# Performance work log

Measured on AMD Instinct MI355X. Metric: run time of the kernel, lower is better.

The kernel has to match this reference:

```python
import jax, jax.numpy as jnp
import numpy as np

C = 256      # channel_num
K = 9        # key_num
B, H, W = 8, 64, 64


def setup_inputs() -> dict:
    key = jax.random.key(0)
    ks = jax.random.split(key, 12)
    s = 1.0 / np.sqrt(C)
    return {
        "query_layer": jax.random.normal(ks[0], (B, C, H, W), jnp.float32),
        "key_layer": jax.random.normal(ks[1], (B, C, H, W), jnp.float32),
        "gumbel_noise": jax.random.gumbel(ks[2], (B, K, H, W), jnp.float32),
        "w_refer": jax.random.normal(ks[3], (C, C), jnp.float32) * s,
        "b_refer": jax.random.normal(ks[4], (C,), jnp.float32) * 0.01,
        "w_attn": jax.random.normal(ks[5], (K, C), jnp.float32) * s,
        "b_attn": jax.random.normal(ks[6], (K,), jnp.float32) * 0.01,
        "w_mask": jax.random.normal(ks[7], (K, C), jnp.float32) * s,
        "b_mask": jax.random.normal(ks[8], (K,), jnp.float32) * 0.01,
        "w_off": jax.random.normal(ks[9], (2 * K, C), jnp.float32) * 0.02,
        "b_off": jax.random.normal(ks[10], (2 * K,), jnp.float32) * 0.01,
        "temp": 1,
    }


def _conv1x1(w, b, x):
    # w: (O,C), x: (B,C,H,W) -> (B,O,H,W)
    return jnp.einsum('oc,bchw->bohw', w, x) + b[None, :, None, None]


def _sample_one(img, py, px):
    # img: (C,H,W); py,px: (K,H,W) absolute sampling coords (bilinear, zero pad)
    h, w = img.shape[1], img.shape[2]
    y0 = jnp.floor(py)
    x0 = jnp.floor(px)
    wy = py - y0          # weight toward y0+1
    wx = px - x0

    def gather(yi, xi):
        valid = (yi >= 0) & (yi < h) & (xi >= 0) & (xi < w)
        yc = jnp.clip(yi, 0, h - 1).astype(jnp.int32)
        xc = jnp.clip(xi, 0, w - 1).astype(jnp.int32)
        return img[:, yc, xc] * valid[None].astype(img.dtype)  # (C,K,H,W)

    out = (gather(y0, x0) * ((1 - wy) * (1 - wx))[None]
           + gather(y0, x0 + 1) * ((1 - wy) * wx)[None]
           + gather(y0 + 1, x0) * (wy * (1 - wx))[None]
           + gather(y0 + 1, x0 + 1) * (wy * wx)[None])
    return out  # (C,K,H,W)


def reference(query_layer, key_layer, gumbel_noise, w_refer, b_refer,
              w_attn, b_attn, w_mask, b_mask, w_off, b_off, temp):
    key_feature = _conv1x1(w_refer, b_refer, key_layer)          # (B,C,H,W)
    attn_weights = _conv1x1(w_attn, b_attn, query_layer)         # (B,K,H,W)
    soft_mask = _conv1x1(w_mask, b_mask, query_layer)            # (B,K,H,W)
    # gumbel_softmax(hard=False) over key dim
    hard_mask = jax.nn.softmax((soft_mask + gumbel_noise) / temp, axis=1)
    offset = _conv1x1(w_off, b_off, query_layer)                 # (B,2K,H,W)

    # faithful to offset[:, i:i+2]: overlapping (dy,dx) slices
    dy = offset[:, 0:K]        # (B,K,H,W)
    dx = offset[:, 1:K + 1]    # (B,K,H,W)
    ys = jnp.arange(H, dtype=offset.dtype)[None, None, :, None]
    xs = jnp.arange(W, dtype=offset.dtype)[None, None, None, :]
    py = ys + dy
    px = xs + dx

    sampled = jax.vmap(_sample_one)(key_feature, py, px)         # (B,C,K,H,W)

    aw = jax.nn.softmax(attn_weights * hard_mask, axis=1)        # (B,K,H,W)
    out = jnp.einsum('bkhw,bckhw->bchw', aw, sampled)            # (B,C,H,W)
    return out
```

## Files before the change

kernel.cpp:

```cpp
#include <hip/hip_runtime.h>

typedef unsigned short u16;
typedef __attribute__((ext_vector_type(8))) short bf16x8;
typedef __attribute__((ext_vector_type(4))) float f32x4;

__device__ __forceinline__ u16 f2bf(float f) {
    unsigned u = __float_as_uint(f);
    unsigned r = (u + 0x7fffu + ((u >> 16) & 1u)) >> 16;
    return (u16)r;
}
__device__ __forceinline__ float bf2f(u16 h) {
    union { unsigned u; float f; } x; x.u = ((unsigned)h) << 16; return x.f;
}

#define NB 8
#define NC 256
#define NK 9
#define NH 64
#define NW 64
#define NP 4096
#define BAND 320
#define SB_STRIDE 328
#define KS_STRIDE 264

__global__ __launch_bounds__(256) void kf_gemm(const float* __restrict__ key,
                                               const float* __restrict__ w_refer,
                                               const float* __restrict__ b_refer,
                                               u16* __restrict__ kf16)
{
    __shared__ u16 K_s[64 * KS_STRIDE];
    const int bid = blockIdx.x;
    const int b   = bid >> 6;
    const int p0  = (bid & 63) << 6;
    const int t = threadIdx.x;
    const int lane = t & 63, wid = t >> 6;
    const int fr = lane & 15, kq = (lane >> 4) << 3;
    const int co0w = wid << 6;

    #pragma unroll
    for (int rep = 0; rep < 16; ++rep) {
        int k = (rep << 4) + (t >> 4), px4 = (t & 15) << 2;
        float4 v = *(const float4*)&key[((size_t)b * NC + k) * NP + p0 + px4];
        K_s[(px4 + 0) * KS_STRIDE + k] = f2bf(v.x);
        K_s[(px4 + 1) * KS_STRIDE + k] = f2bf(v.y);
        K_s[(px4 + 2) * KS_STRIDE + k] = f2bf(v.z);
        K_s[(px4 + 3) * KS_STRIDE + k] = f2bf(v.w);
    }
    __syncthreads();

    f32x4 acc[4][4];
    #pragma unroll
    for (int i = 0; i < 4; ++i)
        #pragma unroll
        for (int j = 0; j < 4; ++j) acc[i][j] = (f32x4){0.f, 0.f, 0.f, 0.f};

    for (int ks = 0; ks < 8; ++ks) {
        const int k0 = (ks << 5) + kq;
        bf16x8 af[4], bfv[4];
        #pragma unroll
        for (int mi = 0; mi < 4; ++mi) {
            const float* src = &w_refer[(size_t)(co0w + (mi << 4) + fr) * NC + k0];
            float4 v0 = *(const float4*)src;
            float4 v1 = *(const float4*)(src + 4);
            bf16x8 a;
            a[0] = (short)f2bf(v0.x); a[1] = (short)f2bf(v0.y);
            a[2] = (short)f2bf(v0.z); a[3] = (short)f2bf(v0.w);
            a[4] = (short)f2bf(v1.x); a[5] = (short)f2bf(v1.y);
            a[6] = (short)f2bf(v1.z); a[7] = (short)f2bf(v1.w);
            af[mi] = a;
        }
        #pragma unroll
        for (int ni = 0; ni < 4; ++ni)
            bfv[ni] = *(const bf16x8*)&K_s[((ni << 4) + fr) * KS_STRIDE + k0];
        #pragma unroll
        for (int mi = 0; mi < 4; ++mi)
            #pragma unroll
            for (int ni = 0; ni < 4; ++ni)
                acc[mi][ni] = __builtin_amdgcn_mfma_f32_16x16x32_bf16(af[mi], bfv[ni], acc[mi][ni], 0, 0, 0);
    }
    const int col = lane & 15, rbase = (lane >> 4) << 2;
    #pragma unroll
    for (int mi = 0; mi < 4; ++mi) {
        #pragma unroll
        for (int rr = 0; rr < 4; ++rr) {
            int co = co0w + (mi << 4) + rbase + rr;
            float bias = b_refer[co];
            u16* dst = &kf16[((size_t)b * NC + co) * NP + p0 + col];
            #pragma unroll
            for (int ni = 0; ni < 4; ++ni)
                dst[ni << 4] = f2bf(acc[mi][ni][rr] + bias);
        }
    }
}

__global__ __launch_bounds__(256) void head_meta(const float* __restrict__ query,
                                                 const float* __restrict__ gumbel,
                                                 const float* __restrict__ w_attn, const float* __restrict__ b_attn,
                                                 const float* __restrict__ w_mask, const float* __restrict__ b_mask,
                                                 const float* __restrict__ w_off,  const float* __restrict__ b_off,
                                                 const int* __restrict__ temp_p,
                                                 float4* __restrict__ wgt, uint2* __restrict__ offs)
{
    __shared__ u16 A[48][264];
    __shared__ float hdT[128][41];
    const int pt = blockIdx.x;
    const int b  = pt >> 5;
    const int p0 = (pt & 31) << 7;
    const int t = threadIdx.x;
    const int lane = t & 63, wn = t >> 6;
    const int fr = lane & 15, kq = (lane >> 4) << 3;

    for (int i = t; i < 1152; i += 256) {
        int o = i >> 5, c = (i & 31) << 3;
        const float* src = (o < 9) ? &w_attn[o * NC + c]
                       : (o < 18 ? &w_mask[(o - 9) * NC + c]
                                 : &w_off[(o - 18) * NC + c]);
        float4 v0 = *(const float4*)src;
        float4 v1 = *(const float4*)(src + 4);
        bf16x8 a;
        a[0] = (short)f2bf(v0.x); a[1] = (short)f2bf(v0.y);
        a[2] = (short)f2bf(v0.z); a[3] = (short)f2bf(v0.w);
        a[4] = (short)f2bf(v1.x); a[5] = (short)f2bf(v1.y);
        a[6] = (short)f2bf(v1.z); a[7] = (short)f2bf(v1.w);
        *(bf16x8*)&A[o][c] = a;
    }
    for (int i = t; i < 384; i += 256) {
        bf16x8 z = {0,0,0,0,0,0,0,0};
        *(bf16x8*)&A[36 + (i >> 5)][(i & 31) << 3] = z;
    }
    __syncthreads();

    f32x4 acc[3][2];
    #pragma unroll
    for (int i = 0; i < 3; ++i)
        #pragma unroll
        for (int j = 0; j < 2; ++j) acc[i][j] = (f32x4){0.f, 0.f, 0.f, 0.f};

    for (int ks = 0; ks < 8; ++ks) {
        const int k0 = (ks << 5) + kq;
        bf16x8 af[3], bfv[2];
        #pragma unroll
        for (int mi = 0; mi < 3; ++mi)
            af[mi] = *(const bf16x8*)&A[(mi << 4) + fr][k0];
        #pragma unroll
        for (int ni = 0; ni < 2; ++ni) {
            const float* src = &query[((size_t)b * NC + k0) * NP + p0 + (wn << 5) + (ni << 4) + fr];
            bf16x8 bv;
            #pragma unroll
            for (int j = 0; j < 8; ++j) bv[j] = (short)f2bf(src[(size_t)j * NP]);
            bfv[ni] = bv;
        }
        #pragma unroll
        for (int mi = 0; mi < 3; ++mi)
            #pragma unroll
            for (int ni = 0; ni < 2; ++ni)
                acc[mi][ni] = __builtin_amdgcn_mfma_f32_16x16x32_bf16(af[mi], bfv[ni], acc[mi][ni], 0, 0, 0);
    }
    const int col = lane & 15, rbase = (lane >> 4) << 2;
    #pragma unroll
    for (int mi = 0; mi < 3; ++mi) {
        #pragma unroll
        for (int rr = 0; rr < 4; ++rr) {
            int o = (mi << 4) + rbase + rr;
            if (o < 36) {
                float bias = (o < 9) ? b_attn[o] : (o < 18) ? b_mask[o - 9] : b_off[o - 18];
                #pragma unroll
                for (int ni = 0; ni < 2; ++ni)
                    hdT[(wn << 5) + (ni << 4) + col][o] = acc[mi][ni][rr] + bias;
            }
        }
    }
    __syncthreads();

    if (t < 128) {
        const int pxg = p0 + t;
        const int row = pxg >> 6, xcol = pxg & 63;
        float v[36];
        #pragma unroll
        for (int o = 0; o < 36; ++o) v[o] = hdT[t][o];

        int ti = temp_p[0];
        float tempf = (ti >= 1 && ti < (1 << 23)) ? (float)ti : __int_as_float(ti);
        float am[9], hs[9];
        float mx = -1e30f;
        #pragma unroll
        for (int k = 0; k < 9; ++k) {
            am[k] = v[k];
            float g = gumbel[((size_t)b * NK + k) * NP + pxg];
            hs[k] = (v[9 + k] + g) / tempf;
            mx = fmaxf(mx, hs[k]);
        }
        float ssum = 0.f;
        #pragma unroll
        for (int k = 0; k < 9; ++k) { hs[k] = __expf(hs[k] - mx); ssum += hs[k]; }
        float inv = 1.f / ssum;
        float lg[9]; float mx2 = -1e30f;
        #pragma unroll
        for (int k = 0; k < 9; ++k) { lg[k] = am[k] * (hs[k] * inv); mx2 = fmaxf(mx2, lg[k]); }
        float s2 = 0.f;
        #pragma unroll
        for (int k = 0; k < 9; ++k) { lg[k] = __expf(lg[k] - mx2); s2 += lg[k]; }
        float inv2 = 1.f / s2;
        #pragma unroll
        for (int k = 0; k < 9; ++k) {
            float a = lg[k] * inv2;
            float pyv = (float)row  + v[18 + k];
            float pxv = (float)xcol + v[19 + k];
            float y0f = floorf(pyv), x0f = floorf(pxv);
            float wy = pyv - y0f, wx = pxv - x0f;
            int y0 = (int)y0f, x0 = (int)x0f;
            int y1 = y0 + 1, x1 = x0 + 1;
            float vy0 = (y0 >= 0 && y0 < NH) ? 1.f : 0.f;
            float vy1 = (y1 >= 0 && y1 < NH) ? 1.f : 0.f;
            float vx0 = (x0 >= 0 && x0 < NW) ? 1.f : 0.f;
            float vx1 = (x1 >= 0 && x1 < NW) ? 1.f : 0.f;
            int y0c = min(max(y0, 0), NH - 1), y1c = min(max(y1, 0), NH - 1);
            int x0c = min(max(x0, 0), NW - 1), x1c = min(max(x1, 0), NW - 1);
            unsigned o00 = (unsigned)(y0c * NW + x0c), o01 = (unsigned)(y0c * NW + x1c);
            unsigned o10 = (unsigned)(y1c * NW + x0c), o11 = (unsigned)(y1c * NW + x1c);
            size_t idx = ((size_t)b * NK + k) * NP + pxg;
            wgt[idx]  = make_float4(a * (1.f - wy) * (1.f - wx) * vy0 * vx0,
                                    a * (1.f - wy) * wx * vy0 * vx1,
                                    a * wy * (1.f - wx) * vy1 * vx0,
                                    a * wy * wx * vy1 * vx1);
            offs[idx] = make_uint2(o00 | (o01 << 16), o10 | (o11 << 16));
        }
    }
}

__global__ __launch_bounds__(512, 4) void sample_pass(const u16* __restrict__ kf16,
                                                      const float4* __restrict__ wgt,
                                                      const uint2* __restrict__ offs,
                                                      float* __restrict__ out)
{
    __shared__ float Sf[64][BAND];

    const int bid = blockIdx.x;
    const int b = bid & 7, row = bid >> 3;
    const int t = threadIdx.x;
    const int lane = t & 63, wid = t >> 6;
    const int fr = lane & 15, kq = (lane >> 4) << 3;
    const int c0 = wid << 5;
    const int ylo = min(max(row - 2, 0), NH - 5);
    const int base = ylo << 6;
    const u16* kfb = kf16 + (size_t)b * NC * NP + base;

    const int px = t & 63, kg = t >> 6;
    size_t idx0 = ((size_t)b * NK + kg) * NP + (row << 6) + px;
    float4 wv0 = wgt[idx0];
    uint2  ov0 = offs[idx0];
    float4 wv1 = make_float4(0.f, 0.f, 0.f, 0.f);
    uint2  ov1 = make_uint2(0u, 0u);
    if (kg == 0) {
        size_t idx1 = ((size_t)b * NK + 8) * NP + (row << 6) + px;
        wv1 = wgt[idx1]; ov1 = offs[idx1];
    }

    #pragma unroll
    for (int i = 0; i < 10; ++i)
        ((float4*)Sf)[t + (i << 9)] = (float4){0.f, 0.f, 0.f, 0.f};
    __syncthreads();

    bool esc = false;
    #pragma unroll
    for (int s = 0; s < 2; ++s) {
        if (s == 1 && kg != 0) break;
        float4 wv = s ? wv1 : wv0;
        uint2  ov = s ? ov1 : ov0;
        int   o4[4] = { (int)(ov.x & 0xffffu), (int)(ov.x >> 16),
                        (int)(ov.y & 0xffffu), (int)(ov.y >> 16) };
        float w4[4] = { wv.x, wv.y, wv.z, wv.w };
        #pragma unroll
        for (int c = 0; c < 4; ++c) {
            int u = o4[c] - base;
            if ((unsigned)u < (unsigned)BAND) atomicAdd(&Sf[px][u], w4[c]);
            else esc = true;
        }
    }
    __syncthreads();

    bf16x8 apre[4][2];
    #pragma unroll
    for (int s = 0; s < 4; ++s)
        #pragma unroll
        for (int mi = 0; mi < 2; ++mi)
            apre[s][mi] = *(const bf16x8*)&kfb[(size_t)(c0 + (mi << 4) + fr) * NP + (s << 5) + kq];

    u16* Sb = (u16*)&Sf[0][0];
    #pragma unroll
    for (int r = 0; r < 5; ++r) {
        int i = t + (r << 9);
        int p = i / 40, j = (i % 40) << 3;
        float4 a = *(const float4*)&Sf[p][j];
        float4 c = *(const float4*)&Sf[p][j + 4];
        bf16x8 q;
        q[0] = (short)f2bf(a.x); q[1] = (short)f2bf(a.y);
        q[2] = (short)f2bf(a.z); q[3] = (short)f2bf(a.w);
        q[4] = (short)f2bf(c.x); q[5] = (short)f2bf(c.y);
        q[6] = (short)f2bf(c.z); q[7] = (short)f2bf(c.w);
        __syncthreads();
        *(bf16x8*)&Sb[p * SB_STRIDE + j] = q;
    }
    __syncthreads();

    f32x4 acc[2][4];
    #pragma unroll
    for (int i = 0; i < 2; ++i)
        #pragma unroll
        for (int j = 0; j < 4; ++j) acc[i][j] = (f32x4){0.f, 0.f, 0.f, 0.f};

    #pragma unroll
    for (int step = 0; step < 10; ++step) {
        bf16x8 a0 = apre[step & 3][0], a1 = apre[step & 3][1];
        if (step + 4 < 10) {
            #pragma unroll
            for (int mi = 0; mi < 2; ++mi)
                apre[step & 3][mi] =
                    *(const bf16x8*)&kfb[(size_t)(c0 + (mi << 4) + fr) * NP + ((step + 4) << 5) + kq];
        }
        bf16x8 bfv[4];
        #pragma unroll
        for (int ni = 0; ni < 4; ++ni)
            bfv[ni] = *(const bf16x8*)&Sb[((ni << 4) + fr) * SB_STRIDE + (step << 5) + kq];
        #pragma unroll
        for (int ni = 0; ni < 4; ++ni) {
            acc[0][ni] = __builtin_amdgcn_mfma_f32_16x16x32_bf16(a0, bfv[ni], acc[0][ni], 0, 0, 0);
            acc[1][ni] = __builtin_amdgcn_mfma_f32_16x16x32_bf16(a1, bfv[ni], acc[1][ni], 0, 0, 0);
        }
    }

    const int col = lane & 15, rbase = (lane >> 4) << 2;
    float* ob = out + (size_t)b * NC * NP + (row << 6);
    #pragma unroll
    for (int mi = 0; mi < 2; ++mi) {
        #pragma unroll
        for (int rr = 0; rr < 4; ++rr) {
            int c = c0 + (mi << 4) + rbase + rr;
            #pragma unroll
            for (int ni = 0; ni < 4; ++ni)
                ob[(size_t)c * NP + (ni << 4) + col] = acc[mi][ni][rr];
        }
    }

    __syncthreads();
    if (esc) {
        for (int s = 0; s < (kg == 0 ? 2 : 1); ++s) {
            int k = s ? 8 : kg;
            size_t idx = ((size_t)b * NK + k) * NP + (row << 6) + px;
            float4 wv = wgt[idx];
            uint2  ov = offs[idx];
            int   o4[4] = { (int)(ov.x & 0xffffu), (int)(ov.x >> 16),
                            (int)(ov.y & 0xffffu), (int)(ov.y >> 16) };
            float w4[4] = { wv.x, wv.y, wv.z, wv.w };
            for (int c = 0; c < 4; ++c) {
                int u = o4[c] - base;
                if ((unsigned)u >= (unsigned)BAND) {
                    for (int cc = 0; cc < NC; ++cc)
                        atomicAdd(&ob[(size_t)cc * NP + px],
                                  w4[c] * bf2f(kf16[((size_t)b * NC + cc) * NP + o4[c]]));
                }
            }
        }
    }
}

extern "C" void kernel_launch(void* const* d_in, const int* in_sizes, int n_in,
                              void* d_out, int out_size, void* d_ws, size_t ws_size,
                              hipStream_t stream)
{
    const float* query   = (const float*)d_in[0];
    const float* key     = (const float*)d_in[1];
    const float* gumbel  = (const float*)d_in[2];
    const float* w_refer = (const float*)d_in[3];
    const float* b_refer = (const float*)d_in[4];
    const float* w_attn  = (const float*)d_in[5];
    const float* b_attn  = (const float*)d_in[6];
    const float* w_mask  = (const float*)d_in[7];
    const float* b_mask  = (const float*)d_in[8];
    const float* w_off   = (const float*)d_in[9];
    const float* b_off   = (const float*)d_in[10];
    const int*   temp    = (const int*)d_in[11];
    float* out = (float*)d_out;

    u16*    kf16 = (u16*)d_ws;
    float4* wgt  = (float4*)((char*)d_ws + (size_t)NB * NP * NC * 2);
    uint2*  offs = (uint2*)((char*)wgt + (size_t)NB * NK * NP * 16);

    kf_gemm<<<512, 256, 0, stream>>>(key, w_refer, b_refer, kf16);
    head_meta<<<256, 256, 0, stream>>>(query, gumbel, w_attn, b_attn, w_mask, b_mask,
                                       w_off, b_off, temp, wgt, offs);
    sample_pass<<<512, 512, 0, stream>>>(kf16, wgt, offs, out);
}
```

Before: 62.10 us.

## Drop LDS staging in kf_gemm, reorder block indexing, hoist prefetch, batch LDS repack

kf_gemm now reads key values straight from global memory into MFMA B fragments with strided scalar loads, removing the LDS transpose and its barrier. Block indices in kf_gemm and head_meta are remapped so consecutive blocks cover different batches. In sample_pass the kf16 A-fragment prefetch moves ahead of the scatter phase, and the bf16 repack collects all five chunks in registers before a single barrier instead of one barrier per chunk. The strided uncoalesced global reads in kf_gemm risk much lower memory efficiency, and the extra live registers may reduce occupancy.

```diff
diff --git a/kernel.cpp b/kernel.cpp
--- a/kernel.cpp
+++ b/kernel.cpp
@@ -21,38 +21,26 @@
 #define NP 4096
 #define BAND 320
 #define SB_STRIDE 328
-#define KS_STRIDE 264
 
 __global__ __launch_bounds__(256) void kf_gemm(const float* __restrict__ key,
                                                const float* __restrict__ w_refer,
                                                const float* __restrict__ b_refer,
                                                u16* __restrict__ kf16)
 {
-    __shared__ u16 K_s[64 * KS_STRIDE];
     const int bid = blockIdx.x;
-    const int b   = bid >> 6;
-    const int p0  = (bid & 63) << 6;
-    const int t = threadIdx.x;
-    const int lane = t & 63, wid = t >> 6;
+    const int b   = bid & 7;
+    const int p0  = (bid >> 3) << 6;
+    const int lane = threadIdx.x & 63, wid = threadIdx.x >> 6;
     const int fr = lane & 15, kq = (lane >> 4) << 3;
     const int co0w = wid << 6;
 
-    #pragma unroll
-    for (int rep = 0; rep < 16; ++rep) {
-        int k = (rep << 4) + (t >> 4), px4 = (t & 15) << 2;
-        float4 v = *(const float4*)&key[((size_t)b * NC + k) * NP + p0 + px4];
-        K_s[(px4 + 0) * KS_STRIDE + k] = f2bf(v.x);
-        K_s[(px4 + 1) * KS_STRIDE + k] = f2bf(v.y);
-        K_s[(px4 + 2) * KS_STRIDE + k] = f2bf(v.z);
-        K_s[(px4 + 3) * KS_STRIDE + k] = f2bf(v.w);
-    }
-    __syncthreads();
-
     f32x4 acc[4][4];
     #pragma unroll
     for (int i = 0; i < 4; ++i)
         #pragma unroll
         for (int j = 0; j < 4; ++j) acc[i][j] = (f32x4){0.f, 0.f, 0.f, 0.f};
+
+    const float* kb = &key[(size_t)b * NC * NP + p0];
 
     for (int ks = 0; ks < 8; ++ks) {
         const int k0 = (ks << 5) + kq;
@@ -70,14 +58,20 @@
             af[mi] = a;
         }
         #pragma unroll
-        for (int ni = 0; ni < 4; ++ni)
-            bfv[ni] = *(const bf16x8*)&K_s[((ni << 4) + fr) * KS_STRIDE + k0];
+        for (int ni = 0; ni < 4; ++ni) {
+            const float* src = &kb[(size_t)k0 * NP + (ni << 4) + fr];
+            bf16x8 bv;
+            #pragma unroll
+            for (int j = 0; j < 8; ++j) bv[j] = (short)f2bf(src[(size_t)j * NP]);
+            bfv[ni] = bv;
+        }
         #pragma unroll
         for (int mi = 0; mi < 4; ++mi)
             #pragma unroll
             for (int ni = 0; ni < 4; ++ni)
                 acc[mi][ni] = __builtin_amdgcn_mfma_f32_16x16x32_bf16(af[mi], bfv[ni], acc[mi][ni], 0, 0, 0);
     }
+
     const int col = lane & 15, rbase = (lane >> 4) << 2;
     #pragma unroll
     for (int mi = 0; mi < 4; ++mi) {
@@ -104,8 +98,8 @@
     __shared__ u16 A[48][264];
     __shared__ float hdT[128][41];
     const int pt = blockIdx.x;
-    const int b  = pt >> 5;
-    const int p0 = (pt & 31) << 7;
+    const int b  = pt & 7;
+    const int p0 = (pt >> 3) << 7;
     const int t = threadIdx.x;
     const int lane = t & 63, wn = t >> 6;
     const int fr = lane & 15, kq = (lane >> 4) << 3;
@@ -245,6 +239,13 @@
     const int base = ylo << 6;
     const u16* kfb = kf16 + (size_t)b * NC * NP + base;
 
+    bf16x8 apre[4][2];
+    #pragma unroll
+    for (int s = 0; s < 4; ++s)
+        #pragma unroll
+        for (int mi = 0; mi < 2; ++mi)
+            apre[s][mi] = *(const bf16x8*)&kfb[(size_t)(c0 + (mi << 4) + fr) * NP + (s << 5) + kq];
+
     const int px = t & 63, kg = t >> 6;
     size_t idx0 = ((size_t)b * NK + kg) * NP + (row << 6) + px;
     float4 wv0 = wgt[idx0];
@@ -279,14 +280,8 @@
     }
     __syncthreads();
 
-    bf16x8 apre[4][2];
-    #pragma unroll
-    for (int s = 0; s < 4; ++s)
-        #pragma unroll
-        for (int mi = 0; mi < 2; ++mi)
-            apre[s][mi] = *(const bf16x8*)&kfb[(size_t)(c0 + (mi << 4) + fr) * NP + (s << 5) + kq];
-
     u16* Sb = (u16*)&Sf[0][0];
+    bf16x8 pk[5]; int po[5];
     #pragma unroll
     for (int r = 0; r < 5; ++r) {
         int i = t + (r << 9);
@@ -298,9 +293,12 @@
         q[2] = (short)f2bf(a.z); q[3] = (short)f2bf(a.w);
         q[4] = (short)f2bf(c.x); q[5] = (short)f2bf(c.y);
         q[6] = (short)f2bf(c.z); q[7] = (short)f2bf(c.w);
-        __syncthreads();
-        *(bf16x8*)&Sb[p * SB_STRIDE + j] = q;
-    }
+        pk[r] = q; po[r] = p * SB_STRIDE + j;
+    }
+    __syncthreads();
+    #pragma unroll
+    for (int r = 0; r < 5; ++r)
+        *(bf16x8*)&Sb[po[r]] = pk[r];
     __syncthreads();
 
     f32x4 acc[2][4];
@@ -382,8 +380,9 @@
     const int*   temp    = (const int*)d_in[11];
     float* out = (float*)d_out;
 
-    u16*    kf16 = (u16*)d_ws;
-    float4* wgt  = (float4*)((char*)d_ws + (size_t)NB * NP * NC * 2);
+    char* ws = (char*)d_ws;
+    u16*    kf16 = (u16*)ws;
+    float4* wgt  = (float4*)(ws + (size_t)NB * NP * NC * 2);
     uint2*  offs = (uint2*)((char*)wgt + (size_t)NB * NK * NP * 16);
 
     kf_gemm<<<512, 256, 0, stream>>>(key, w_refer, b_refer, kf16);
```

After: 67.16 us. 8.2% more time.
